# Kernel tuning notes

Hardware: AMD Instinct MI355X
Metric: run time of the kernel (lower is better)

## Reference

```python
import jax, jax.numpy as jnp
import numpy as np

N_NODES = 100000
N_EDGES = 3200000
IN_DIM = 128
HID = 64


def setup_inputs() -> dict:
    key = jax.random.key(0)
    ks = jax.random.split(key, 6)
    x = jax.random.normal(ks[0], (N_NODES, IN_DIM), dtype=jnp.float32)
    edge_index = jax.random.randint(ks[1], (2, N_EDGES), 0, N_NODES, dtype=jnp.int64)
    s1 = 1.0 / np.sqrt(IN_DIM)
    s2 = 1.0 / np.sqrt(HID)
    W1_l = jax.random.normal(ks[2], (IN_DIM, HID), dtype=jnp.float32) * s1
    W1_r = jax.random.normal(ks[3], (IN_DIM, HID), dtype=jnp.float32) * s1
    b1 = jnp.zeros((HID,), dtype=jnp.float32)
    W2_l = jax.random.normal(ks[4], (HID, 1), dtype=jnp.float32) * s2
    W2_r = jax.random.normal(ks[5], (HID, 1), dtype=jnp.float32) * s2
    b2 = jnp.zeros((1,), dtype=jnp.float32)
    return {"x": x, "edge_index": edge_index, "W1_l": W1_l, "b1": b1,
            "W1_r": W1_r, "W2_l": W2_l, "b2": b2, "W2_r": W2_r}


def _sage_conv(h, src, dst, deg_inv, W_l, b, W_r):
    # PyG SAGEConv (mean aggr): lin_l(mean_{j in N(i)} h_j) + lin_r(h_i)
    agg = jax.ops.segment_sum(h[src], dst, num_segments=h.shape[0])  # [N, d]
    agg = agg * deg_inv[:, None]
    return agg @ W_l + b + h @ W_r


def reference(x, edge_index, W1_l, b1, W1_r, W2_l, b2, W2_r):
    src, dst = edge_index[0], edge_index[1]
    n = x.shape[0]
    deg = jax.ops.segment_sum(jnp.ones_like(src, dtype=x.dtype), dst, num_segments=n)
    deg_inv = jnp.where(deg > 0, 1.0 / jnp.maximum(deg, 1.0), 0.0)
    h = jax.nn.relu(_sage_conv(x, src, dst, deg_inv, W1_l, b1, W1_r))
    out = _sage_conv(h, src, dst, deg_inv, W2_l, b2, W2_r)  # [N, 1]
    return jax.nn.sigmoid(out).squeeze(-1)  # [N]
```

## Files before the change

### kernel.cpp

```cpp
#include <hip/hip_runtime.h>
#include <math.h>

#define N_NODES 100000
#define N_EDGES 3200000
#define IN_DIM  128
#define HID     64
#define N_MTILE (N_NODES / 16)

#define E_BLK    4096
#define NBLK_BIN ((N_EDGES + E_BLK - 1) / E_BLK)
#define BUCKETS  500
#define BRANGE   200
#define CAP      8192
#define CAPG     8192

typedef unsigned int  uint;
typedef unsigned short ushort_t;
typedef __attribute__((ext_vector_type(8))) short bf16x8;
typedef __attribute__((ext_vector_type(4))) float f32x4;

__device__ __forceinline__ uint cvtpk(float lo, float hi) {
    uint r;
    asm("v_cvt_pk_bf16_f32 %0, %1, %2" : "=v"(r) : "v"(lo), "v"(hi));
    return r;
}

__global__ __launch_bounds__(256) void wrepack(const float* __restrict__ Wl,
                                               const float* __restrict__ Wr,
                                               ushort_t* __restrict__ wpk) {
    const int idx = blockIdx.x * 256 + threadIdx.x;
    if (idx >= 128 * 128) return;
    const int j = idx & 7;
    const int l = (idx >> 3) & 63;
    const int s = (idx >> 9) & 3;
    const int t = idx >> 11;
    const int row = s * 32 + ((l >> 4) << 3) + j;
    const int col = t * 16 + (l & 15);
    const float v = (col < 64) ? Wl[row * 64 + col] : Wr[row * 64 + (col - 64)];
    uint a = __float_as_uint(v);
    a = (a + 0x7fffu + ((a >> 16) & 1u)) >> 16;
    wpk[idx] = (ushort_t)a;
}

__global__ __launch_bounds__(256) void gemm1m(const float* __restrict__ x,
                                              const ushort_t* __restrict__ wpk,
                                              const float* __restrict__ b1,
                                              uint* __restrict__ xlb,
                                              uint* __restrict__ xrb) {
    __shared__ float ax[16][132];
    const int tid  = threadIdx.x;
    const int wid  = tid >> 6;
    const int lane = tid & 63;
    const int t0   = wid * 2;
    const int r16  = lane & 15;
    const int kg   = lane >> 4;

    bf16x8 bf[2][4];
    #pragma unroll
    for (int tt = 0; tt < 2; ++tt)
        #pragma unroll
        for (int s = 0; s < 4; ++s)
            bf[tt][s] = *(const bf16x8*)&wpk[(((size_t)(t0 + tt) * 4 + s) * 64 + lane) * 8];

    float bias[2] = {0.f, 0.f};
    if (wid >= 2) {
        bias[0] = b1[(t0 + 0) * 16 + r16 - 64];
        bias[1] = b1[(t0 + 1) * 16 + r16 - 64];
    }

    const int row0 = blockIdx.x * 16;

    {
        const int r = tid >> 5;
        const int o = tid & 31;
        #pragma unroll
        for (int it = 0; it < 2; ++it) {
            const int rr = it * 8 + r;
            const f32x4 g = __builtin_nontemporal_load(
                (const f32x4*)&x[(size_t)(row0 + rr) * IN_DIM + o * 4]);
            *(f32x4*)&ax[rr][o * 4] = g;
        }
    }
    __syncthreads();

    f32x4 acc[2];
    acc[0] = (f32x4){0.f, 0.f, 0.f, 0.f};
    acc[1] = (f32x4){0.f, 0.f, 0.f, 0.f};

    #pragma unroll
    for (int s = 0; s < 4; ++s) {
        const float* lp = &ax[r16][s * 32 + kg * 8];
        const f32x4 a0 = *(const f32x4*)lp;
        const f32x4 a1 = *(const f32x4*)(lp + 4);
        union { uint u[4]; bf16x8 v; } af;
        af.u[0] = cvtpk(a0.x, a0.y);
        af.u[1] = cvtpk(a0.z, a0.w);
        af.u[2] = cvtpk(a1.x, a1.y);
        af.u[3] = cvtpk(a1.z, a1.w);
        acc[0] = __builtin_amdgcn_mfma_f32_16x16x32_bf16(af.v, bf[0][s], acc[0], 0, 0, 0);
        acc[1] = __builtin_amdgcn_mfma_f32_16x16x32_bf16(af.v, bf[1][s], acc[1], 0, 0, 0);
    }

    uint* outp = (wid < 2) ? xlb : xrb;
    #pragma unroll
    for (int tt = 0; tt < 2; ++tt) {
        const int colL = ((wid < 2) ? (t0 + tt) : (t0 + tt - 4)) * 16 + r16;
        #pragma unroll
        for (int r = 0; r < 4; ++r) {
            const float mine  = acc[tt][r] + bias[tt];
            const float other = __shfl_xor(mine, 1);
            if ((lane & 1) == 0) {
                const int row = row0 + kg * 4 + r;
                outp[(size_t)row * 32 + (colL >> 1)] = cvtpk(mine, other);
            }
        }
    }
}

__global__ __launch_bounds__(256) void binScatter2(const int* __restrict__ ei,
                                                   int* __restrict__ gcur,
                                                   uint* __restrict__ pairs) {
    __shared__ int      hcnt[BUCKETS];
    __shared__ int      lbase[BUCKETS + 1];
    __shared__ int      dbase[BUCKETS];
    __shared__ ushort_t bktof[E_BLK];
    __shared__ uint     staged[E_BLK];
    __shared__ int      sc[256];

    const int tid = threadIdx.x;
    const int e0  = blockIdx.x * E_BLK;
    const int e1  = min(e0 + E_BLK, N_EDGES);
    const int n   = e1 - e0;

    for (int j = tid; j < BUCKETS; j += 256) hcnt[j] = 0;
    __syncthreads();

    uint pk[16]; int bk[16]; int rk[16];
    #pragma unroll
    for (int k = 0; k < 16; ++k) {
        const int e = e0 + k * 256 + tid;
        pk[k] = 0; bk[k] = -1; rk[k] = 0;
        if (e < e1) {
            const int dst = __builtin_nontemporal_load(&ei[N_EDGES + e]);
            const int src = __builtin_nontemporal_load(&ei[e]);
            const int bkt = dst / BRANGE;
            pk[k] = ((uint)(dst - bkt * BRANGE) << 17) | (uint)src;
            bk[k] = bkt;
            rk[k] = atomicAdd(&hcnt[bkt], 1);
        }
    }
    __syncthreads();

    {
        int v0 = 0, v1 = 0;
        if (tid < 250) { v0 = hcnt[2 * tid]; v1 = hcnt[2 * tid + 1]; }
        const int s = v0 + v1;
        sc[tid] = s;
        __syncthreads();
        for (int off = 1; off < 256; off <<= 1) {
            int t = (tid >= off) ? sc[tid - off] : 0;
            __syncthreads();
            sc[tid] += t;
            __syncthreads();
        }
        const int excl = sc[tid] - s;
        if (tid < 250) {
            lbase[2 * tid]     = excl;
            lbase[2 * tid + 1] = excl + v0;
        }
        if (tid == 0) lbase[BUCKETS] = n;
    }
    __syncthreads();

    for (int j = tid; j < BUCKETS; j += 256) {
        const int c = hcnt[j];
        int resv = 0;
        if (c > 0) resv = atomicAdd(&gcur[j], c);
        dbase[j] = j * CAPG + resv - lbase[j];
    }
    __syncthreads();

    #pragma unroll
    for (int k = 0; k < 16; ++k) {
        if (bk[k] >= 0) staged[lbase[bk[k]] + rk[k]] = pk[k];
    }
    for (int j = tid; j < BUCKETS; j += 256) {
        const int t1 = lbase[j + 1];
        for (int t = lbase[j]; t < t1; ++t) bktof[t] = (ushort_t)j;
    }
    __syncthreads();

    for (int t = tid; t < n; t += 256) {
        const int j    = bktof[t];
        const int dest = dbase[j] + t;
        if (dest < (j + 1) * CAPG)
            __builtin_nontemporal_store(staged[t], &pairs[dest]);
    }
}

__global__ __launch_bounds__(1024) void agg1bucket(const uint* __restrict__ pairs,
                                                   const int* __restrict__ gcur,
                                                   const uint2* __restrict__ xlb2,
                                                   const uint2* __restrict__ xrb2,
                                                   const float* __restrict__ w2l,
                                                   const float* __restrict__ w2r,
                                                   const float* __restrict__ b2,
                                                   float* __restrict__ hl,
                                                   float* __restrict__ hr,
                                                   float* __restrict__ deg_inv) {
    __shared__ int  h[BRANGE];
    __shared__ int  sstart[BRANGE];
    __shared__ int  curs[BRANGE];
    __shared__ int  sc[256];
    __shared__ uint lsrc[CAP];

    const int tid  = threadIdx.x;
    const int wid  = tid >> 6;
    const int lane = tid & 63;
    const int b    = blockIdx.x;
    const int n0   = b * BRANGE;

    for (int i = tid; i < BRANGE; i += 1024) h[i] = 0;
    __syncthreads();

    const int bs = b * CAPG;
    const int be = bs + min(gcur[b], CAPG);

    for (int e = bs + tid; e < be; e += 1024)
        atomicAdd(&h[pairs[e] >> 17], 1);
    __syncthreads();

    {
        int v = 0;
        if (tid < 256) { v = (tid < BRANGE) ? h[tid] : 0; sc[tid] = v; }
        __syncthreads();
        for (int off = 1; off < 256; off <<= 1) {
            int t = 0;
            if (tid < 256 && tid >= off) t = sc[tid - off];
            __syncthreads();
            if (tid < 256) sc[tid] += t;
            __syncthreads();
        }
        if (tid < BRANGE) {
            const int ex = sc[tid] - h[tid];
            sstart[tid] = ex;
            curs[tid]   = ex;
        }
    }
    __syncthreads();

    for (int e = bs + tid; e < be; e += 1024) {
        const uint p = pairs[e];
        const int r = atomicAdd(&curs[p >> 17], 1);
        if (r < CAP) lsrc[r] = p & 0x1FFFFu;
    }
    __syncthreads();

    const int es = lane >> 4;
    const int u  = lane & 15;
    for (int nn = wid; nn < BRANGE; nn += 16) {
        const int st = sstart[nn];
        const int c  = h[nn];

        float a0 = 0.f, a1 = 0.f, a2 = 0.f, a3 = 0.f;
        for (int jj = 0; jj < c; jj += 32) {
            uint2 v[8];
            #pragma unroll
            for (int q = 0; q < 8; ++q) {
                const int idx = jj + q * 4 + es;
                const uint sp = lsrc[st + (idx < c ? idx : 0)];
                if (idx < c) v[q] = xlb2[(size_t)sp * 16 + u];
                else         v[q] = make_uint2(0u, 0u);
            }
            #pragma unroll
            for (int q = 0; q < 8; ++q) {
                a0 += __uint_as_float(v[q].x << 16);
                a1 += __uint_as_float(v[q].x & 0xffff0000u);
                a2 += __uint_as_float(v[q].y << 16);
                a3 += __uint_as_float(v[q].y & 0xffff0000u);
            }
        }
        a0 += __shfl_xor(a0, 16); a1 += __shfl_xor(a1, 16);
        a2 += __shfl_xor(a2, 16); a3 += __shfl_xor(a3, 16);
        a0 += __shfl_xor(a0, 32); a1 += __shfl_xor(a1, 32);
        a2 += __shfl_xor(a2, 32); a3 += __shfl_xor(a3, 32);

        const int node = n0 + nn;
        const float di = (c > 0) ? (1.0f / (float)c) : 0.f;
        const uint2 xv = xrb2[(size_t)node * 16 + u];
        const float x0 = __uint_as_float(xv.x << 16);
        const float x1 = __uint_as_float(xv.x & 0xffff0000u);
        const float x2 = __uint_as_float(xv.y << 16);
        const float x3 = __uint_as_float(xv.y & 0xffff0000u);
        const float h0 = fmaxf(a0 * di + x0, 0.f);
        const float h1 = fmaxf(a1 * di + x1, 0.f);
        const float h2 = fmaxf(a2 * di + x2, 0.f);
        const float h3 = fmaxf(a3 * di + x3, 0.f);
        const f32x4 wl = *(const f32x4*)&w2l[4 * u];
        const f32x4 wr = *(const f32x4*)&w2r[4 * u];
        float a  = h0 * wl.x + h1 * wl.y + h2 * wl.z + h3 * wl.w;
        float bb = h0 * wr.x + h1 * wr.y + h2 * wr.z + h3 * wr.w;
        a += __shfl_xor(a, 1); bb += __shfl_xor(bb, 1);
        a += __shfl_xor(a, 2); bb += __shfl_xor(bb, 2);
        a += __shfl_xor(a, 4); bb += __shfl_xor(bb, 4);
        a += __shfl_xor(a, 8); bb += __shfl_xor(bb, 8);

        if (lane == 0) {
            hl[node]      = a;
            hr[node]      = bb + b2[0];
            deg_inv[node] = di;
        }
    }
}

__global__ __launch_bounds__(512) void aggL2bucket(const uint* __restrict__ pairs,
                                                   const int* __restrict__ gcur,
                                                   const float* __restrict__ hl,
                                                   const float* __restrict__ hr,
                                                   const float* __restrict__ deg_inv,
                                                   float* __restrict__ out) {
    __shared__ float acc2[BRANGE];
    const int tid = threadIdx.x;
    const int b   = blockIdx.x;
    const int n0  = b * BRANGE;

    for (int i = tid; i < BRANGE; i += 512) acc2[i] = 0.f;
    __syncthreads();

    const int bs = b * CAPG;
    const int be = bs + min(gcur[b], CAPG);

    for (int e = bs + tid; e < be; e += 512) {
        const uint p = __builtin_nontemporal_load(&pairs[e]);
        atomicAdd(&acc2[p >> 17], hl[p & 0x1FFFFu]);
    }
    __syncthreads();

    if (tid < BRANGE) {
        const int node = n0 + tid;
        const float z = acc2[tid] * deg_inv[node] + hr[node];
        out[node] = 1.0f / (1.0f + expf(-z));
    }
}

extern "C" void kernel_launch(void* const* d_in, const int* in_sizes, int n_in,
                              void* d_out, int out_size, void* d_ws, size_t ws_size,
                              hipStream_t stream) {
    const float* x    = (const float*)d_in[0];
    const int*   ei   = (const int*)  d_in[1];
    const float* W1l  = (const float*)d_in[2];
    const float* b1   = (const float*)d_in[3];
    const float* W1r  = (const float*)d_in[4];
    const float* W2l  = (const float*)d_in[5];
    const float* b2   = (const float*)d_in[6];
    const float* W2r  = (const float*)d_in[7];
    float* out = (float*)d_out;

    char* wsb = (char*)d_ws;
    const size_t N = N_NODES;
    uint*     xlb     = (uint*)wsb;      wsb += 32 * N * 4;
    uint*     xrb     = (uint*)wsb;      wsb += 32 * N * 4;
    float*    hl      = (float*)wsb;     wsb += N * 4;
    float*    hr      = (float*)wsb;     wsb += N * 4;
    float*    deg_inv = (float*)wsb;     wsb += N * 4;
    int*      gcur    = (int*)wsb;       wsb += 512 * 4;
    uint*     pairs   = (uint*)wsb;      wsb += (size_t)BUCKETS * CAPG * 4;
    ushort_t* wpk     = (ushort_t*)wsb;  wsb += 128 * 128 * 2;

    hipMemsetAsync(gcur, 0, 512 * sizeof(int), stream);

    wrepack<<<64, 256, 0, stream>>>(W1l, W1r, wpk);
    gemm1m<<<N_MTILE, 256, 0, stream>>>(x, wpk, b1, xlb, xrb);

    binScatter2<<<NBLK_BIN, 256, 0, stream>>>(ei, gcur, pairs);

    agg1bucket<<<BUCKETS, 1024, 0, stream>>>(pairs, gcur,
                                             (const uint2*)xlb, (const uint2*)xrb,
                                             W2l, W2r, b2, hl, hr, deg_inv);
    aggL2bucket<<<BUCKETS, 512, 0, stream>>>(pairs, gcur,
                                             hl, hr, deg_inv, out);
}
```

Before: 150.0 us.

## Fold gcur memset into wrepack, widen gathers, per-wave histograms, vectorize layer-2 loads

Replaces the separate memset launch by zeroing gcur inside wrepack, cutting one launch. binScatter2 keeps a shared-memory histogram per wave so fewer threads contend on the same atomic counters. agg1bucket gathers 16-byte bf16 rows (8 lanes per neighbor instead of 16) to issue fewer, wider loads. aggL2bucket uses 1024 threads and reads edge pairs as 4-wide vectors. The extra per-wave offset pass adds a little shared-memory work.

```diff
diff --git a/kernel.cpp b/kernel.cpp
--- a/kernel.cpp
+++ b/kernel.cpp
@@ -18,6 +18,8 @@
 typedef unsigned short ushort_t;
 typedef __attribute__((ext_vector_type(8))) short bf16x8;
 typedef __attribute__((ext_vector_type(4))) float f32x4;
+typedef __attribute__((ext_vector_type(2))) float f32x2;
+typedef __attribute__((ext_vector_type(4))) uint  u32x4;
 
 __device__ __forceinline__ uint cvtpk(float lo, float hi) {
     uint r;
@@ -27,7 +29,12 @@
 
 __global__ __launch_bounds__(256) void wrepack(const float* __restrict__ Wl,
                                                const float* __restrict__ Wr,
-                                               ushort_t* __restrict__ wpk) {
+                                               ushort_t* __restrict__ wpk,
+                                               int* __restrict__ gcur) {
+    if (blockIdx.x < 2) {
+        const int g = blockIdx.x * 256 + threadIdx.x;
+        if (g < 512) gcur[g] = 0;
+    }
     const int idx = blockIdx.x * 256 + threadIdx.x;
     if (idx >= 128 * 128) return;
     const int j = idx & 7;
@@ -120,7 +127,8 @@
 __global__ __launch_bounds__(256) void binScatter2(const int* __restrict__ ei,
                                                    int* __restrict__ gcur,
                                                    uint* __restrict__ pairs) {
-    __shared__ int      hcnt[BUCKETS];
+    __shared__ int      hcnt[4][BUCKETS];
+    __shared__ int      tot[BUCKETS];
     __shared__ int      lbase[BUCKETS + 1];
     __shared__ int      dbase[BUCKETS];
     __shared__ ushort_t bktof[E_BLK];
@@ -128,11 +136,14 @@
     __shared__ int      sc[256];
 
     const int tid = threadIdx.x;
+    const int w   = tid >> 6;
     const int e0  = blockIdx.x * E_BLK;
     const int e1  = min(e0 + E_BLK, N_EDGES);
     const int n   = e1 - e0;
 
-    for (int j = tid; j < BUCKETS; j += 256) hcnt[j] = 0;
+    for (int j = tid; j < BUCKETS; j += 256) {
+        hcnt[0][j] = 0; hcnt[1][j] = 0; hcnt[2][j] = 0; hcnt[3][j] = 0;
+    }
     __syncthreads();
 
     uint pk[16]; int bk[16]; int rk[16];
@@ -146,14 +157,24 @@
             const int bkt = dst / BRANGE;
             pk[k] = ((uint)(dst - bkt * BRANGE) << 17) | (uint)src;
             bk[k] = bkt;
-            rk[k] = atomicAdd(&hcnt[bkt], 1);
-        }
+            rk[k] = atomicAdd(&hcnt[w][bkt], 1);
+        }
+    }
+    __syncthreads();
+
+    for (int j = tid; j < BUCKETS; j += 256) {
+        const int c0 = hcnt[0][j], c1 = hcnt[1][j], c2 = hcnt[2][j], c3 = hcnt[3][j];
+        hcnt[0][j] = 0;
+        hcnt[1][j] = c0;
+        hcnt[2][j] = c0 + c1;
+        hcnt[3][j] = c0 + c1 + c2;
+        tot[j]     = c0 + c1 + c2 + c3;
     }
     __syncthreads();
 
     {
         int v0 = 0, v1 = 0;
-        if (tid < 250) { v0 = hcnt[2 * tid]; v1 = hcnt[2 * tid + 1]; }
+        if (tid < 250) { v0 = tot[2 * tid]; v1 = tot[2 * tid + 1]; }
         const int s = v0 + v1;
         sc[tid] = s;
         __syncthreads();
@@ -173,7 +194,7 @@
     __syncthreads();
 
     for (int j = tid; j < BUCKETS; j += 256) {
-        const int c = hcnt[j];
+        const int c = tot[j];
         int resv = 0;
         if (c > 0) resv = atomicAdd(&gcur[j], c);
         dbase[j] = j * CAPG + resv - lbase[j];
@@ -182,7 +203,7 @@
 
     #pragma unroll
     for (int k = 0; k < 16; ++k) {
-        if (bk[k] >= 0) staged[lbase[bk[k]] + rk[k]] = pk[k];
+        if (bk[k] >= 0) staged[lbase[bk[k]] + hcnt[w][bk[k]] + rk[k]] = pk[k];
     }
     for (int j = tid; j < BUCKETS; j += 256) {
         const int t1 = lbase[j + 1];
@@ -200,8 +221,8 @@
 
 __global__ __launch_bounds__(1024) void agg1bucket(const uint* __restrict__ pairs,
                                                    const int* __restrict__ gcur,
-                                                   const uint2* __restrict__ xlb2,
-                                                   const uint2* __restrict__ xrb2,
+                                                   const u32x4* __restrict__ xlb4,
+                                                   const u32x4* __restrict__ xrb4,
                                                    const float* __restrict__ w2l,
                                                    const float* __restrict__ w2r,
                                                    const float* __restrict__ b2,
@@ -256,54 +277,64 @@
     }
     __syncthreads();
 
-    const int es = lane >> 4;
-    const int u  = lane & 15;
+    const int es = lane >> 3;
+    const int u  = lane & 7;
     for (int nn = wid; nn < BRANGE; nn += 16) {
         const int st = sstart[nn];
         const int c  = h[nn];
 
-        float a0 = 0.f, a1 = 0.f, a2 = 0.f, a3 = 0.f;
+        f32x2 A0 = {0.f, 0.f}, A1 = {0.f, 0.f}, A2 = {0.f, 0.f}, A3 = {0.f, 0.f};
         for (int jj = 0; jj < c; jj += 32) {
-            uint2 v[8];
+            u32x4 v[4];
             #pragma unroll
-            for (int q = 0; q < 8; ++q) {
-                const int idx = jj + q * 4 + es;
+            for (int q = 0; q < 4; ++q) {
+                const int idx = jj + q * 8 + es;
                 const uint sp = lsrc[st + (idx < c ? idx : 0)];
-                if (idx < c) v[q] = xlb2[(size_t)sp * 16 + u];
-                else         v[q] = make_uint2(0u, 0u);
+                if (idx < c) v[q] = xlb4[(sp << 3) + u];
+                else         v[q] = (u32x4){0u, 0u, 0u, 0u};
             }
             #pragma unroll
-            for (int q = 0; q < 8; ++q) {
-                a0 += __uint_as_float(v[q].x << 16);
-                a1 += __uint_as_float(v[q].x & 0xffff0000u);
-                a2 += __uint_as_float(v[q].y << 16);
-                a3 += __uint_as_float(v[q].y & 0xffff0000u);
+            for (int q = 0; q < 4; ++q) {
+                A0 += (f32x2){__uint_as_float(v[q].x << 16),
+                              __uint_as_float(v[q].x & 0xffff0000u)};
+                A1 += (f32x2){__uint_as_float(v[q].y << 16),
+                              __uint_as_float(v[q].y & 0xffff0000u)};
+                A2 += (f32x2){__uint_as_float(v[q].z << 16),
+                              __uint_as_float(v[q].z & 0xffff0000u)};
+                A3 += (f32x2){__uint_as_float(v[q].w << 16),
+                              __uint_as_float(v[q].w & 0xffff0000u)};
             }
         }
-        a0 += __shfl_xor(a0, 16); a1 += __shfl_xor(a1, 16);
-        a2 += __shfl_xor(a2, 16); a3 += __shfl_xor(a3, 16);
-        a0 += __shfl_xor(a0, 32); a1 += __shfl_xor(a1, 32);
-        a2 += __shfl_xor(a2, 32); a3 += __shfl_xor(a3, 32);
+        #pragma unroll
+        for (int off = 8; off <= 32; off <<= 1) {
+            A0.x += __shfl_xor(A0.x, off); A0.y += __shfl_xor(A0.y, off);
+            A1.x += __shfl_xor(A1.x, off); A1.y += __shfl_xor(A1.y, off);
+            A2.x += __shfl_xor(A2.x, off); A2.y += __shfl_xor(A2.y, off);
+            A3.x += __shfl_xor(A3.x, off); A3.y += __shfl_xor(A3.y, off);
+        }
 
         const int node = n0 + nn;
         const float di = (c > 0) ? (1.0f / (float)c) : 0.f;
-        const uint2 xv = xrb2[(size_t)node * 16 + u];
-        const float x0 = __uint_as_float(xv.x << 16);
-        const float x1 = __uint_as_float(xv.x & 0xffff0000u);
-        const float x2 = __uint_as_float(xv.y << 16);
-        const float x3 = __uint_as_float(xv.y & 0xffff0000u);
-        const float h0 = fmaxf(a0 * di + x0, 0.f);
-        const float h1 = fmaxf(a1 * di + x1, 0.f);
-        const float h2 = fmaxf(a2 * di + x2, 0.f);
-        const float h3 = fmaxf(a3 * di + x3, 0.f);
-        const f32x4 wl = *(const f32x4*)&w2l[4 * u];
-        const f32x4 wr = *(const f32x4*)&w2r[4 * u];
-        float a  = h0 * wl.x + h1 * wl.y + h2 * wl.z + h3 * wl.w;
-        float bb = h0 * wr.x + h1 * wr.y + h2 * wr.z + h3 * wr.w;
+        const u32x4 xv = xrb4[((uint)node << 3) + u];
+        const float h0 = fmaxf(A0.x * di + __uint_as_float(xv.x << 16), 0.f);
+        const float h1 = fmaxf(A0.y * di + __uint_as_float(xv.x & 0xffff0000u), 0.f);
+        const float h2 = fmaxf(A1.x * di + __uint_as_float(xv.y << 16), 0.f);
+        const float h3 = fmaxf(A1.y * di + __uint_as_float(xv.y & 0xffff0000u), 0.f);
+        const float h4 = fmaxf(A2.x * di + __uint_as_float(xv.z << 16), 0.f);
+        const float h5 = fmaxf(A2.y * di + __uint_as_float(xv.z & 0xffff0000u), 0.f);
+        const float h6 = fmaxf(A3.x * di + __uint_as_float(xv.w << 16), 0.f);
+        const float h7 = fmaxf(A3.y * di + __uint_as_float(xv.w & 0xffff0000u), 0.f);
+        const f32x4 wl0 = *(const f32x4*)&w2l[8 * u];
+        const f32x4 wl1 = *(const f32x4*)&w2l[8 * u + 4];
+        const f32x4 wr0 = *(const f32x4*)&w2r[8 * u];
+        const f32x4 wr1 = *(const f32x4*)&w2r[8 * u + 4];
+        float a  = h0 * wl0.x + h1 * wl0.y + h2 * wl0.z + h3 * wl0.w
+                 + h4 * wl1.x + h5 * wl1.y + h6 * wl1.z + h7 * wl1.w;
+        float bb = h0 * wr0.x + h1 * wr0.y + h2 * wr0.z + h3 * wr0.w
+                 + h4 * wr1.x + h5 * wr1.y + h6 * wr1.z + h7 * wr1.w;
         a += __shfl_xor(a, 1); bb += __shfl_xor(bb, 1);
         a += __shfl_xor(a, 2); bb += __shfl_xor(bb, 2);
         a += __shfl_xor(a, 4); bb += __shfl_xor(bb, 4);
-        a += __shfl_xor(a, 8); bb += __shfl_xor(bb, 8);
 
         if (lane == 0) {
             hl[node]      = a;
@@ -313,26 +344,37 @@
     }
 }
 
-__global__ __launch_bounds__(512) void aggL2bucket(const uint* __restrict__ pairs,
-                                                   const int* __restrict__ gcur,
-                                                   const float* __restrict__ hl,
-                                                   const float* __restrict__ hr,
-                                                   const float* __restrict__ deg_inv,
-                                                   float* __restrict__ out) {
+__global__ __launch_bounds__(1024) void aggL2bucket(const uint* __restrict__ pairs,
+                                                    const int* __restrict__ gcur,
+                                                    const float* __restrict__ hl,
+                                                    const float* __restrict__ hr,
+                                                    const float* __restrict__ deg_inv,
+                                                    float* __restrict__ out) {
     __shared__ float acc2[BRANGE];
     const int tid = threadIdx.x;
     const int b   = blockIdx.x;
     const int n0  = b * BRANGE;
 
-    for (int i = tid; i < BRANGE; i += 512) acc2[i] = 0.f;
-    __syncthreads();
-
-    const int bs = b * CAPG;
-    const int be = bs + min(gcur[b], CAPG);
-
-    for (int e = bs + tid; e < be; e += 512) {
-        const uint p = __builtin_nontemporal_load(&pairs[e]);
-        atomicAdd(&acc2[p >> 17], hl[p & 0x1FFFFu]);
+    if (tid < BRANGE) acc2[tid] = 0.f;
+    __syncthreads();
+
+    const int bs  = b * CAPG;
+    const int cnt = min(gcur[b], CAPG);
+    const u32x4* p4 = (const u32x4*)(pairs + bs);
+    const int n4 = (cnt + 3) >> 2;
+
+    for (int i = tid; i < n4; i += 1024) {
+        const u32x4 pv = __builtin_nontemporal_load(&p4[i]);
+        const int base = i * 4;
+        float g0 = 0.f, g1 = 0.f, g2 = 0.f, g3 = 0.f;
+        if (base + 0 < cnt) g0 = hl[pv.x & 0x1FFFFu];
+        if (base + 1 < cnt) g1 = hl[pv.y & 0x1FFFFu];
+        if (base + 2 < cnt) g2 = hl[pv.z & 0x1FFFFu];
+        if (base + 3 < cnt) g3 = hl[pv.w & 0x1FFFFu];
+        if (base + 0 < cnt) atomicAdd(&acc2[pv.x >> 17], g0);
+        if (base + 1 < cnt) atomicAdd(&acc2[pv.y >> 17], g1);
+        if (base + 2 < cnt) atomicAdd(&acc2[pv.z >> 17], g2);
+        if (base + 3 < cnt) atomicAdd(&acc2[pv.w >> 17], g3);
     }
     __syncthreads();
 
@@ -367,16 +409,14 @@
     uint*     pairs   = (uint*)wsb;      wsb += (size_t)BUCKETS * CAPG * 4;
     ushort_t* wpk     = (ushort_t*)wsb;  wsb += 128 * 128 * 2;
 
-    hipMemsetAsync(gcur, 0, 512 * sizeof(int), stream);
-
-    wrepack<<<64, 256, 0, stream>>>(W1l, W1r, wpk);
+    wrepack<<<64, 256, 0, stream>>>(W1l, W1r, wpk, gcur);
     gemm1m<<<N_MTILE, 256, 0, stream>>>(x, wpk, b1, xlb, xrb);
 
     binScatter2<<<NBLK_BIN, 256, 0, stream>>>(ei, gcur, pairs);
 
     agg1bucket<<<BUCKETS, 1024, 0, stream>>>(pairs, gcur,
-                                             (const uint2*)xlb, (const uint2*)xrb,
+                                             (const u32x4*)xlb, (const u32x4*)xrb,
                                              W2l, W2r, b2, hl, hr, deg_inv);
-    aggL2bucket<<<BUCKETS, 512, 0, stream>>>(pairs, gcur,
-                                             hl, hr, deg_inv, out);
-}
+    aggL2bucket<<<BUCKETS, 1024, 0, stream>>>(pairs, gcur,
+                                              hl, hr, deg_inv, out);
+}
```

Measured after the change: 155.7 us. 1.04x slower.

## Use per-wave histograms in binning, vectorize layer-2 gather, fold memset into repack

Applied to the files above, without the earlier changes.

The binning kernel now processes 8192 edges per 512-thread block and keeps a separate LDS histogram per wave, then turns them into per-wave prefix offsets, which is meant to cut LDS atomic contention. The layer-2 aggregation kernel runs 1024 threads and loads four packed pairs per thread as one 128-bit load, issuing the gathers before the atomics to gain memory-level parallelism. The gcur zeroing moves from a separate memset into the weight-repack kernel, removing one launch. The trade-offs are more LDS per binning block (lower occupancy) and extra bounds checks in the layer-2 kernel.

```diff
diff --git a/kernel.cpp b/kernel.cpp
--- a/kernel.cpp
+++ b/kernel.cpp
@@ -7,7 +7,7 @@
 #define HID     64
 #define N_MTILE (N_NODES / 16)
 
-#define E_BLK    4096
+#define E_BLK    8192
 #define NBLK_BIN ((N_EDGES + E_BLK - 1) / E_BLK)
 #define BUCKETS  500
 #define BRANGE   200
@@ -18,6 +18,7 @@
 typedef unsigned short ushort_t;
 typedef __attribute__((ext_vector_type(8))) short bf16x8;
 typedef __attribute__((ext_vector_type(4))) float f32x4;
+typedef __attribute__((ext_vector_type(4))) uint  u32x4;
 
 __device__ __forceinline__ uint cvtpk(float lo, float hi) {
     uint r;
@@ -27,7 +28,12 @@
 
 __global__ __launch_bounds__(256) void wrepack(const float* __restrict__ Wl,
                                                const float* __restrict__ Wr,
-                                               ushort_t* __restrict__ wpk) {
+                                               ushort_t* __restrict__ wpk,
+                                               int* __restrict__ gcur) {
+    if (blockIdx.x < 2) {
+        const int g = blockIdx.x * 256 + threadIdx.x;
+        if (g < 512) gcur[g] = 0;
+    }
     const int idx = blockIdx.x * 256 + threadIdx.x;
     if (idx >= 128 * 128) return;
     const int j = idx & 7;
@@ -117,10 +123,11 @@
     }
 }
 
-__global__ __launch_bounds__(256) void binScatter2(const int* __restrict__ ei,
+__global__ __launch_bounds__(512) void binScatter2(const int* __restrict__ ei,
                                                    int* __restrict__ gcur,
                                                    uint* __restrict__ pairs) {
-    __shared__ int      hcnt[BUCKETS];
+    __shared__ int      hcnt[8][BUCKETS];
+    __shared__ int      tot[BUCKETS];
     __shared__ int      lbase[BUCKETS + 1];
     __shared__ int      dbase[BUCKETS];
     __shared__ ushort_t bktof[E_BLK];
@@ -128,17 +135,21 @@
     __shared__ int      sc[256];
 
     const int tid = threadIdx.x;
+    const int w   = tid >> 6;
     const int e0  = blockIdx.x * E_BLK;
     const int e1  = min(e0 + E_BLK, N_EDGES);
     const int n   = e1 - e0;
 
-    for (int j = tid; j < BUCKETS; j += 256) hcnt[j] = 0;
+    for (int j = tid; j < BUCKETS; j += 512) {
+        #pragma unroll
+        for (int q = 0; q < 8; ++q) hcnt[q][j] = 0;
+    }
     __syncthreads();
 
     uint pk[16]; int bk[16]; int rk[16];
     #pragma unroll
     for (int k = 0; k < 16; ++k) {
-        const int e = e0 + k * 256 + tid;
+        const int e = e0 + k * 512 + tid;
         pk[k] = 0; bk[k] = -1; rk[k] = 0;
         if (e < e1) {
             const int dst = __builtin_nontemporal_load(&ei[N_EDGES + e]);
@@ -146,25 +157,37 @@
             const int bkt = dst / BRANGE;
             pk[k] = ((uint)(dst - bkt * BRANGE) << 17) | (uint)src;
             bk[k] = bkt;
-            rk[k] = atomicAdd(&hcnt[bkt], 1);
-        }
+            rk[k] = atomicAdd(&hcnt[w][bkt], 1);
+        }
+    }
+    __syncthreads();
+
+    for (int j = tid; j < BUCKETS; j += 512) {
+        int run = 0;
+        #pragma unroll
+        for (int q = 0; q < 8; ++q) {
+            const int c = hcnt[q][j];
+            hcnt[q][j] = run;
+            run += c;
+        }
+        tot[j] = run;
     }
     __syncthreads();
 
     {
-        int v0 = 0, v1 = 0;
-        if (tid < 250) { v0 = hcnt[2 * tid]; v1 = hcnt[2 * tid + 1]; }
-        const int s = v0 + v1;
-        sc[tid] = s;
+        int v0 = 0, v1 = 0, s = 0;
+        if (tid < 250) { v0 = tot[2 * tid]; v1 = tot[2 * tid + 1]; }
+        if (tid < 256) { s = v0 + v1; sc[tid] = s; }
         __syncthreads();
         for (int off = 1; off < 256; off <<= 1) {
-            int t = (tid >= off) ? sc[tid - off] : 0;
+            int t = 0;
+            if (tid < 256 && tid >= off) t = sc[tid - off];
             __syncthreads();
-            sc[tid] += t;
+            if (tid < 256) sc[tid] += t;
             __syncthreads();
         }
-        const int excl = sc[tid] - s;
         if (tid < 250) {
+            const int excl = sc[tid] - s;
             lbase[2 * tid]     = excl;
             lbase[2 * tid + 1] = excl + v0;
         }
@@ -172,8 +195,8 @@
     }
     __syncthreads();
 
-    for (int j = tid; j < BUCKETS; j += 256) {
-        const int c = hcnt[j];
+    for (int j = tid; j < BUCKETS; j += 512) {
+        const int c = tot[j];
         int resv = 0;
         if (c > 0) resv = atomicAdd(&gcur[j], c);
         dbase[j] = j * CAPG + resv - lbase[j];
@@ -182,15 +205,15 @@
 
     #pragma unroll
     for (int k = 0; k < 16; ++k) {
-        if (bk[k] >= 0) staged[lbase[bk[k]] + rk[k]] = pk[k];
-    }
-    for (int j = tid; j < BUCKETS; j += 256) {
+        if (bk[k] >= 0) staged[lbase[bk[k]] + hcnt[w][bk[k]] + rk[k]] = pk[k];
+    }
+    for (int j = tid; j < BUCKETS; j += 512) {
         const int t1 = lbase[j + 1];
         for (int t = lbase[j]; t < t1; ++t) bktof[t] = (ushort_t)j;
     }
     __syncthreads();
 
-    for (int t = tid; t < n; t += 256) {
+    for (int t = tid; t < n; t += 512) {
         const int j    = bktof[t];
         const int dest = dbase[j] + t;
         if (dest < (j + 1) * CAPG)
@@ -313,26 +336,37 @@
     }
 }
 
-__global__ __launch_bounds__(512) void aggL2bucket(const uint* __restrict__ pairs,
-                                                   const int* __restrict__ gcur,
-                                                   const float* __restrict__ hl,
-                                                   const float* __restrict__ hr,
-                                                   const float* __restrict__ deg_inv,
-                                                   float* __restrict__ out) {
+__global__ __launch_bounds__(1024) void aggL2bucket(const uint* __restrict__ pairs,
+                                                    const int* __restrict__ gcur,
+                                                    const float* __restrict__ hl,
+                                                    const float* __restrict__ hr,
+                                                    const float* __restrict__ deg_inv,
+                                                    float* __restrict__ out) {
     __shared__ float acc2[BRANGE];
     const int tid = threadIdx.x;
     const int b   = blockIdx.x;
     const int n0  = b * BRANGE;
 
-    for (int i = tid; i < BRANGE; i += 512) acc2[i] = 0.f;
-    __syncthreads();
-
-    const int bs = b * CAPG;
-    const int be = bs + min(gcur[b], CAPG);
-
-    for (int e = bs + tid; e < be; e += 512) {
-        const uint p = __builtin_nontemporal_load(&pairs[e]);
-        atomicAdd(&acc2[p >> 17], hl[p & 0x1FFFFu]);
+    if (tid < BRANGE) acc2[tid] = 0.f;
+    __syncthreads();
+
+    const int bs  = b * CAPG;
+    const int cnt = min(gcur[b], CAPG);
+    const u32x4* p4 = (const u32x4*)(pairs + bs);
+    const int n4 = (cnt + 3) >> 2;
+
+    for (int i = tid; i < n4; i += 1024) {
+        const u32x4 pv = __builtin_nontemporal_load(&p4[i]);
+        const int base = i * 4;
+        float g0 = 0.f, g1 = 0.f, g2 = 0.f, g3 = 0.f;
+        if (base + 0 < cnt) g0 = hl[pv.x & 0x1FFFFu];
+        if (base + 1 < cnt) g1 = hl[pv.y & 0x1FFFFu];
+        if (base + 2 < cnt) g2 = hl[pv.z & 0x1FFFFu];
+        if (base + 3 < cnt) g3 = hl[pv.w & 0x1FFFFu];
+        if (base + 0 < cnt) atomicAdd(&acc2[pv.x >> 17], g0);
+        if (base + 1 < cnt) atomicAdd(&acc2[pv.y >> 17], g1);
+        if (base + 2 < cnt) atomicAdd(&acc2[pv.z >> 17], g2);
+        if (base + 3 < cnt) atomicAdd(&acc2[pv.w >> 17], g3);
     }
     __syncthreads();
 
@@ -367,16 +401,14 @@
     uint*     pairs   = (uint*)wsb;      wsb += (size_t)BUCKETS * CAPG * 4;
     ushort_t* wpk     = (ushort_t*)wsb;  wsb += 128 * 128 * 2;
 
-    hipMemsetAsync(gcur, 0, 512 * sizeof(int), stream);
-
-    wrepack<<<64, 256, 0, stream>>>(W1l, W1r, wpk);
+    wrepack<<<64, 256, 0, stream>>>(W1l, W1r, wpk, gcur);
     gemm1m<<<N_MTILE, 256, 0, stream>>>(x, wpk, b1, xlb, xrb);
 
-    binScatter2<<<NBLK_BIN, 256, 0, stream>>>(ei, gcur, pairs);
+    binScatter2<<<NBLK_BIN, 512, 0, stream>>>(ei, gcur, pairs);
 
     agg1bucket<<<BUCKETS, 1024, 0, stream>>>(pairs, gcur,
                                              (const uint2*)xlb, (const uint2*)xrb,
                                              W2l, W2r, b2, hl, hr, deg_inv);
-    aggL2bucket<<<BUCKETS, 512, 0, stream>>>(pairs, gcur,
-                                             hl, hr, deg_inv, out);
-}
+    aggL2bucket<<<BUCKETS, 1024, 0, stream>>>(pairs, gcur,
+                                              hl, hr, deg_inv, out);
+}
```

Result: faster. 138.5 us (median of 2 runs) (-7.6%).
